# Kernel optimization log

Measured on AMD Instinct MI355X. Metric: run time of the kernel, lower is better.

## Reference

```python
import jax, jax.numpy as jnp
import numpy as np

P = 1_500_000
N_DEPTH = 6 * 118 * 16 * 44  # 498432 flattened depth bins
N_FEAT = 6 * 16 * 44         # 4224 flattened feature rows
TOTAL_BEV = 40000            # 200x200 BEV grid
C = 80


def setup_inputs() -> dict:
    key = jax.random.key(0)
    k1, k2, k3, k4, k5, k6, k7 = jax.random.split(key, 7)
    depth = jax.random.uniform(k1, (6, 118, 16, 44), dtype=jnp.float32)
    feat = jax.random.normal(k2, (6, 16, 44, C), dtype=jnp.float32)
    ranks_depth = jax.random.randint(k3, (P,), 0, N_DEPTH, dtype=jnp.int64)
    ranks_feat = jax.random.randint(k4, (P,), 0, N_FEAT, dtype=jnp.int64)
    ranks_bev = jnp.sort(jax.random.randint(k5, (P,), 0, TOTAL_BEV, dtype=jnp.int64))
    interval_starts = jnp.sort(jax.random.randint(k6, (TOTAL_BEV,), 0, P, dtype=jnp.int64))
    interval_lengths = jax.random.randint(k7, (TOTAL_BEV,), 0, 64, dtype=jnp.int64)
    return {
        "depth": depth,
        "feat": feat,
        "ranks_depth": ranks_depth,
        "ranks_feat": ranks_feat,
        "ranks_bev": ranks_bev,
        "interval_starts": interval_starts,
        "interval_lengths": interval_lengths,
        "total_bev": TOTAL_BEV,
    }


def reference(depth, feat, ranks_depth, ranks_feat, ranks_bev,
              interval_starts, interval_lengths, total_bev):
    # interval_starts / interval_lengths are unused (as in the torch source)
    channels = feat.shape[-1]
    feat_flat = feat.reshape(-1, channels).astype(jnp.float32)   # [N_feat, C]
    depth_flat = depth.reshape(-1).astype(jnp.float32)           # [N_depth]
    gathered_feat = feat_flat[ranks_feat]                        # [P, C]
    gathered_depth = depth_flat[ranks_depth][:, None]            # [P, 1]
    weighted_feat = gathered_feat * gathered_depth               # [P, C]
    out = jax.ops.segment_sum(weighted_feat, ranks_bev,
                              num_segments=int(total_bev))       # [total_bev, C]
    return out
```

## Files before the change

kernel.cpp:

```cpp
#include <hip/hip_runtime.h>


#define CHN 80

__global__ __launch_bounds__(256)
void seg_starts_kernel(const int* __restrict__ rb, int* __restrict__ seg,
                       int P, int total_bev) {
    int q = blockIdx.x * blockDim.x + threadIdx.x;
    int i4 = q * 4;
    if (i4 >= P) return;
    const int4 v = *reinterpret_cast<const int4*>(rb + i4);
    int prev = (i4 == 0) ? -1 : rb[i4 - 1];
    int cur;
    cur = v.x; for (int b = prev + 1; b <= cur; ++b) seg[b] = i4 + 0; prev = cur;
    cur = v.y; for (int b = prev + 1; b <= cur; ++b) seg[b] = i4 + 1; prev = cur;
    cur = v.z; for (int b = prev + 1; b <= cur; ++b) seg[b] = i4 + 2; prev = cur;
    cur = v.w; for (int b = prev + 1; b <= cur; ++b) seg[b] = i4 + 3; prev = cur;
    if (i4 + 4 >= P) {
        for (int b = prev + 1; b <= total_bev; ++b) seg[b] = P;
    }
}

__global__ __launch_bounds__(256)
void bev_pool_kernel(const float* __restrict__ depth,
                     const float* __restrict__ feat,
                     const int* __restrict__ rd,
                     const int* __restrict__ rf,
                     const int* __restrict__ seg,
                     float* __restrict__ out,
                     int total_bev) {
    const int wave = threadIdx.x >> 6;
    const int lane = threadIdx.x & 63;
    const int bin = blockIdx.x * 4 + wave;
    if (bin >= total_bev) return;

    const int slot = lane >> 2;
    const int ll   = lane & 3;

    const int lo = seg[bin];
    const int hi = seg[bin + 1];

    float4 a0 = make_float4(0.f, 0.f, 0.f, 0.f);
    float4 a1 = a0, a2 = a0, a3 = a0, a4 = a0;

    int i = lo + slot;
    bool valid = i < hi;
    int di = 0, fi = 0;
    if (valid) { di = rd[i]; fi = rf[i]; }
    while (valid) {
        const int ni = i + 16;
        const bool nvalid = ni < hi;
        int ndi = 0, nfi = 0;
        if (nvalid) { ndi = rd[ni]; nfi = rf[ni]; }

        const float d = depth[di];
        const float4* frow = reinterpret_cast<const float4*>(feat + (size_t)fi * CHN) + ll;
        const float4 f0 = frow[0];
        const float4 f1 = frow[4];
        const float4 f2 = frow[8];
        const float4 f3 = frow[12];
        const float4 f4 = frow[16];
        a0.x += d * f0.x; a0.y += d * f0.y; a0.z += d * f0.z; a0.w += d * f0.w;
        a1.x += d * f1.x; a1.y += d * f1.y; a1.z += d * f1.z; a1.w += d * f1.w;
        a2.x += d * f2.x; a2.y += d * f2.y; a2.z += d * f2.z; a2.w += d * f2.w;
        a3.x += d * f3.x; a3.y += d * f3.y; a3.z += d * f3.z; a3.w += d * f3.w;
        a4.x += d * f4.x; a4.y += d * f4.y; a4.z += d * f4.z; a4.w += d * f4.w;

        i = ni; di = ndi; fi = nfi; valid = nvalid;
    }

    #pragma unroll
    for (int ofs = 4; ofs <= 32; ofs <<= 1) {
        a0.x += __shfl_xor(a0.x, ofs, 64); a0.y += __shfl_xor(a0.y, ofs, 64);
        a0.z += __shfl_xor(a0.z, ofs, 64); a0.w += __shfl_xor(a0.w, ofs, 64);
        a1.x += __shfl_xor(a1.x, ofs, 64); a1.y += __shfl_xor(a1.y, ofs, 64);
        a1.z += __shfl_xor(a1.z, ofs, 64); a1.w += __shfl_xor(a1.w, ofs, 64);
        a2.x += __shfl_xor(a2.x, ofs, 64); a2.y += __shfl_xor(a2.y, ofs, 64);
        a2.z += __shfl_xor(a2.z, ofs, 64); a2.w += __shfl_xor(a2.w, ofs, 64);
        a3.x += __shfl_xor(a3.x, ofs, 64); a3.y += __shfl_xor(a3.y, ofs, 64);
        a3.z += __shfl_xor(a3.z, ofs, 64); a3.w += __shfl_xor(a3.w, ofs, 64);
        a4.x += __shfl_xor(a4.x, ofs, 64); a4.y += __shfl_xor(a4.y, ofs, 64);
        a4.z += __shfl_xor(a4.z, ofs, 64); a4.w += __shfl_xor(a4.w, ofs, 64);
    }

    if (lane < 20) {
        const int j = lane >> 2;
        float4 w = a0;
        if (j == 1) w = a1;
        else if (j == 2) w = a2;
        else if (j == 3) w = a3;
        else if (j == 4) w = a4;
        *reinterpret_cast<float4*>(out + (size_t)bin * CHN + lane * 4) = w;
    }
}

extern "C" void kernel_launch(void* const* d_in, const int* in_sizes, int n_in,
                              void* d_out, int out_size, void* d_ws, size_t ws_size,
                              hipStream_t stream) {
    const float* depth = (const float*)d_in[0];
    const float* feat  = (const float*)d_in[1];
    const int*   rd    = (const int*)d_in[2];
    const int*   rf    = (const int*)d_in[3];
    const int*   rb    = (const int*)d_in[4];
    float* out = (float*)d_out;

    const int P = in_sizes[2];
    const int total_bev = out_size / CHN;

    int* seg = (int*)d_ws;

    const int quads = (P + 3) / 4;
    seg_starts_kernel<<<(quads + 255) / 256, 256, 0, stream>>>(rb, seg, P, total_bev);
    bev_pool_kernel<<<(total_bev + 3) / 4, 256, 0, stream>>>(depth, feat, rd, rf, seg,
                                                             out, total_bev);
}
```

Measured before the change: 119.4 us.

## Convert feature table to fp16 in fused prologue and gather half rows

```diff
diff --git a/kernel.cpp b/kernel.cpp
--- a/kernel.cpp
+++ b/kernel.cpp
@@ -1,7 +1,106 @@
 #include <hip/hip_runtime.h>
+#include <hip/hip_fp16.h>
 
 
 #define CHN 80
+
+__global__ __launch_bounds__(256)
+void prologue_kernel(const int* __restrict__ rb, int* __restrict__ seg,
+                     const float* __restrict__ feat, __half* __restrict__ feat16,
+                     int P, int total_bev, int nfeat) {
+    const int gid = blockIdx.x * blockDim.x + threadIdx.x;
+    if (gid < nfeat) feat16[gid] = __float2half(feat[gid]);
+
+    const int i4 = gid * 4;
+    if (i4 >= P) return;
+    const int4 v = *reinterpret_cast<const int4*>(rb + i4);
+    int prev = (i4 == 0) ? -1 : rb[i4 - 1];
+    int cur;
+    cur = v.x; for (int b = prev + 1; b <= cur; ++b) seg[b] = i4 + 0; prev = cur;
+    cur = v.y; for (int b = prev + 1; b <= cur; ++b) seg[b] = i4 + 1; prev = cur;
+    cur = v.z; for (int b = prev + 1; b <= cur; ++b) seg[b] = i4 + 2; prev = cur;
+    cur = v.w; for (int b = prev + 1; b <= cur; ++b) seg[b] = i4 + 3; prev = cur;
+    if (i4 + 4 >= P) {
+        for (int b = prev + 1; b <= total_bev; ++b) seg[b] = P;
+    }
+}
+
+__device__ __forceinline__ void acc8(float* a, const uint4& u, float d) {
+    const __half2* h = reinterpret_cast<const __half2*>(&u);
+#pragma unroll
+    for (int k = 0; k < 4; ++k) {
+        const float2 f = __half22float2(h[k]);
+        a[2 * k]     += d * f.x;
+        a[2 * k + 1] += d * f.y;
+    }
+}
+
+__global__ __launch_bounds__(256)
+void bev_pool_f16_kernel(const float* __restrict__ depth,
+                         const __half* __restrict__ feat16,
+                         const int* __restrict__ rd,
+                         const int* __restrict__ rf,
+                         const int* __restrict__ seg,
+                         float* __restrict__ out,
+                         int total_bev) {
+    const int wave = threadIdx.x >> 6;
+    const int lane = threadIdx.x & 63;
+    const int bin = blockIdx.x * 4 + wave;
+    if (bin >= total_bev) return;
+
+    const int slot = lane >> 2;
+    const int ll   = lane & 3;
+
+    const int lo = seg[bin];
+    const int hi = seg[bin + 1];
+
+    float a[24];
+#pragma unroll
+    for (int k = 0; k < 24; ++k) a[k] = 0.f;
+
+    int i = lo + slot;
+    bool valid = i < hi;
+    int di = 0, fi = 0;
+    if (valid) { di = rd[i]; fi = rf[i]; }
+    while (valid) {
+        const int ni = i + 16;
+        const bool nvalid = ni < hi;
+        int ndi = 0, nfi = 0;
+        if (nvalid) { ndi = rd[ni]; nfi = rf[ni]; }
+
+        const float d = depth[di];
+        const __half* row = feat16 + (size_t)fi * CHN;
+        const uint4 u0 = *reinterpret_cast<const uint4*>(row + ll * 8);
+        const uint4 u1 = *reinterpret_cast<const uint4*>(row + 32 + ll * 8);
+        uint4 u2 = make_uint4(0u, 0u, 0u, 0u);
+        if (ll < 2) u2 = *reinterpret_cast<const uint4*>(row + 64 + ll * 8);
+
+        acc8(a + 0,  u0, d);
+        acc8(a + 8,  u1, d);
+        acc8(a + 16, u2, d);
+
+        i = ni; di = ndi; fi = nfi; valid = nvalid;
+    }
+
+#pragma unroll
+    for (int ofs = 4; ofs <= 32; ofs <<= 1) {
+#pragma unroll
+        for (int k = 0; k < 24; ++k) a[k] += __shfl_xor(a[k], ofs, 64);
+    }
+
+    float* orow = out + (size_t)bin * CHN;
+    if (lane < 4) {
+        const int b0 = lane * 8;
+        *reinterpret_cast<float4*>(orow + b0)          = make_float4(a[0],  a[1],  a[2],  a[3]);
+        *reinterpret_cast<float4*>(orow + b0 + 4)      = make_float4(a[4],  a[5],  a[6],  a[7]);
+        *reinterpret_cast<float4*>(orow + 32 + b0)     = make_float4(a[8],  a[9],  a[10], a[11]);
+        *reinterpret_cast<float4*>(orow + 36 + b0)     = make_float4(a[12], a[13], a[14], a[15]);
+    } else if (lane < 6) {
+        const int b2 = (lane - 4) * 8;
+        *reinterpret_cast<float4*>(orow + 64 + b2)     = make_float4(a[16], a[17], a[18], a[19]);
+        *reinterpret_cast<float4*>(orow + 68 + b2)     = make_float4(a[20], a[21], a[22], a[23]);
+    }
+}
 
 __global__ __launch_bounds__(256)
 void seg_starts_kernel(const int* __restrict__ rb, int* __restrict__ seg,
@@ -22,27 +121,23 @@
 }
 
 __global__ __launch_bounds__(256)
-void bev_pool_kernel(const float* __restrict__ depth,
-                     const float* __restrict__ feat,
-                     const int* __restrict__ rd,
-                     const int* __restrict__ rf,
-                     const int* __restrict__ seg,
-                     float* __restrict__ out,
-                     int total_bev) {
+void bev_pool_f32_kernel(const float* __restrict__ depth,
+                         const float* __restrict__ feat,
+                         const int* __restrict__ rd,
+                         const int* __restrict__ rf,
+                         const int* __restrict__ seg,
+                         float* __restrict__ out,
+                         int total_bev) {
     const int wave = threadIdx.x >> 6;
     const int lane = threadIdx.x & 63;
     const int bin = blockIdx.x * 4 + wave;
     if (bin >= total_bev) return;
-
     const int slot = lane >> 2;
     const int ll   = lane & 3;
-
     const int lo = seg[bin];
     const int hi = seg[bin + 1];
-
     float4 a0 = make_float4(0.f, 0.f, 0.f, 0.f);
     float4 a1 = a0, a2 = a0, a3 = a0, a4 = a0;
-
     int i = lo + slot;
     bool valid = i < hi;
     int di = 0, fi = 0;
@@ -52,24 +147,17 @@
         const bool nvalid = ni < hi;
         int ndi = 0, nfi = 0;
         if (nvalid) { ndi = rd[ni]; nfi = rf[ni]; }
-
         const float d = depth[di];
         const float4* frow = reinterpret_cast<const float4*>(feat + (size_t)fi * CHN) + ll;
-        const float4 f0 = frow[0];
-        const float4 f1 = frow[4];
-        const float4 f2 = frow[8];
-        const float4 f3 = frow[12];
-        const float4 f4 = frow[16];
+        const float4 f0 = frow[0], f1 = frow[4], f2 = frow[8], f3 = frow[12], f4 = frow[16];
         a0.x += d * f0.x; a0.y += d * f0.y; a0.z += d * f0.z; a0.w += d * f0.w;
         a1.x += d * f1.x; a1.y += d * f1.y; a1.z += d * f1.z; a1.w += d * f1.w;
         a2.x += d * f2.x; a2.y += d * f2.y; a2.z += d * f2.z; a2.w += d * f2.w;
         a3.x += d * f3.x; a3.y += d * f3.y; a3.z += d * f3.z; a3.w += d * f3.w;
         a4.x += d * f4.x; a4.y += d * f4.y; a4.z += d * f4.z; a4.w += d * f4.w;
-
         i = ni; di = ndi; fi = nfi; valid = nvalid;
     }
-
-    #pragma unroll
+#pragma unroll
     for (int ofs = 4; ofs <= 32; ofs <<= 1) {
         a0.x += __shfl_xor(a0.x, ofs, 64); a0.y += __shfl_xor(a0.y, ofs, 64);
         a0.z += __shfl_xor(a0.z, ofs, 64); a0.w += __shfl_xor(a0.w, ofs, 64);
@@ -82,7 +170,6 @@
         a4.x += __shfl_xor(a4.x, ofs, 64); a4.y += __shfl_xor(a4.y, ofs, 64);
         a4.z += __shfl_xor(a4.z, ofs, 64); a4.w += __shfl_xor(a4.w, ofs, 64);
     }
-
     if (lane < 20) {
         const int j = lane >> 2;
         float4 w = a0;
@@ -105,12 +192,27 @@
     float* out = (float*)d_out;
 
     const int P = in_sizes[2];
+    const int nfeat = in_sizes[1];
     const int total_bev = out_size / CHN;
 
+    const size_t seg_bytes = ((size_t)(total_bev + 1) * 4 + 15) & ~(size_t)15;
+    const size_t need = seg_bytes + (size_t)nfeat * 2;
+
     int* seg = (int*)d_ws;
-
     const int quads = (P + 3) / 4;
-    seg_starts_kernel<<<(quads + 255) / 256, 256, 0, stream>>>(rb, seg, P, total_bev);
-    bev_pool_kernel<<<(total_bev + 3) / 4, 256, 0, stream>>>(depth, feat, rd, rf, seg,
-                                                             out, total_bev);
-}
+    const int quad_blocks = (quads + 255) / 256;
+
+    if (ws_size >= need) {
+        __half* feat16 = (__half*)((char*)d_ws + seg_bytes);
+        const int cvt_blocks = (nfeat + 255) / 256;
+        const int pro_blocks = quad_blocks > cvt_blocks ? quad_blocks : cvt_blocks;
+        prologue_kernel<<<pro_blocks, 256, 0, stream>>>(rb, seg, feat, feat16,
+                                                        P, total_bev, nfeat);
+        bev_pool_f16_kernel<<<(total_bev + 3) / 4, 256, 0, stream>>>(
+            depth, feat16, rd, rf, seg, out, total_bev);
+    } else {
+        seg_starts_kernel<<<quad_blocks, 256, 0, stream>>>(rb, seg, P, total_bev);
+        bev_pool_f32_kernel<<<(total_bev + 3) / 4, 256, 0, stream>>>(
+            depth, feat, rd, rf, seg, out, total_bev);
+    }
+}
```

New measurement: 127.2 us. 6.6% more time.
